# Performance work log

Hardware: AMD Instinct MI355X
Metric: run time of the kernel (lower is better)

## Reference

```python
import jax, jax.numpy as jnp
import numpy as np


def setup_inputs() -> dict:
    key = jax.random.key(0)
    k1, k2 = jax.random.split(key)
    B, Lq, Ls, D = 16, 2048, 2048, 512
    query = jax.random.normal(k1, (B, Lq, D), dtype=jnp.float32)
    support = jax.random.normal(k2, (B, Ls, D), dtype=jnp.float32)
    return {"query": query, "support": support}


def reference(query, support):
    # attn: [B, Lq, Ls] = softmax(query @ support^T, axis=-1)
    logits = jnp.einsum("bqd,bsd->bqs", query, support)
    attn = jax.nn.softmax(logits, axis=-1)
    # attended support: [B, Lq, D]
    attended = jnp.einsum("bqs,bsd->bqd", attn, support)
    # score: [B, Lq] = sum over D of query * attended
    score = jnp.sum(query * attended, axis=-1)
    return score
```

## Files before the change

kernel.cpp:

```cpp
#include <hip/hip_runtime.h>
#include <hip/hip_bf16.h>

#define B_  16
#define LQ  2048
#define LS  2048
#define DD  512
#define BQ  128
#define BS  128
#define BK  64
#define NSB (LS / BS)
#define NKC (DD / BK)
#define NSPLIT 4

typedef short bf16x8 __attribute__((ext_vector_type(8)));
typedef float f32x4  __attribute__((ext_vector_type(4)));

__device__ __forceinline__ void load_lds16(const void* g, void* l) {
  __builtin_amdgcn_global_load_lds((const __attribute__((address_space(1))) void*)g,
                                   (__attribute__((address_space(3))) void*)l,
                                   16, 0, 0);
}

__device__ __forceinline__ unsigned short f2bf(float f) {
  union { float f; unsigned int u; } v; v.f = f;
  unsigned int r = v.u + 0x7fffu + ((v.u >> 16) & 1u);
  return (unsigned short)(r >> 16);
}

__global__ __launch_bounds__(256) void cvt_kernel(const float* __restrict__ Q,
                                                  const float* __restrict__ S,
                                                  unsigned short* __restrict__ Qw,
                                                  unsigned short* __restrict__ Sw,
                                                  int nblk) {
  int blk = blockIdx.x;
  const float* src; unsigned short* dst;
  if (blk < nblk) { src = Q; dst = Qw; } else { src = S; dst = Sw; blk -= nblk; }
  int i = blk * 256 + threadIdx.x;
  float4 f = ((const float4*)src)[i];
  ushort4 u;
  u.x = f2bf(f.x); u.y = f2bf(f.y); u.z = f2bf(f.z); u.w = f2bf(f.w);
  ((ushort4*)dst)[i] = u;
}

__global__ __launch_bounds__(512, 4) void attn_kernel(const unsigned short* __restrict__ Qw,
                                                      const unsigned short* __restrict__ Sw,
                                                      float* __restrict__ out,
                                                      float* __restrict__ pm,
                                                      float* __restrict__ pse,
                                                      float* __restrict__ psel,
                                                      int nsplit) {
  __shared__ __align__(16) unsigned short sQ[BQ * BK];
  __shared__ __align__(16) unsigned short sS[BS * BK];

  const int qb   = blockIdx.x;
  const int b    = blockIdx.y;
  const int spl  = blockIdx.z;
  const int tid  = threadIdx.x;
  const int w    = tid >> 6;
  const int lane = tid & 63;
  const int h    = w & 1;
  const int g    = w >> 1;
  const int col  = lane & 15;
  const int quad = lane >> 4;
  const int c7   = col & 7;

  const int q0 = qb * BQ;
  const unsigned short* Qb = Qw + (size_t)b * LQ * DD;
  const unsigned short* Sb = Sw + (size_t)b * LS * DD;

  float mst[2] = { -INFINITY, -INFINITY };
  float se[2]  = { 0.f, 0.f };
  float sel[2] = { 0.f, 0.f };

  f32x4 acc[4][2];

  const int rr    = lane >> 3;
  const int cc    = ((lane & 7) ^ rr) * 8;
  const int srow0 = (w & 3) * 32;

  const int sbs = spl * (NSB / nsplit);
  const int sbe = sbs + (NSB / nsplit);

  for (int sb = sbs; sb < sbe; ++sb) {
    const int s0 = sb * BS;
#pragma unroll
    for (int st = 0; st < 4; ++st)
#pragma unroll
      for (int qt = 0; qt < 2; ++qt)
        acc[st][qt] = (f32x4){0.f, 0.f, 0.f, 0.f};

    for (int kc = 0; kc < NKC; ++kc) {
      __syncthreads();
      if (w < 4) {
#pragma unroll
        for (int i = 0; i < 4; ++i) {
          int r = srow0 + i * 8 + rr;
          load_lds16(Qb + (size_t)(q0 + r) * DD + kc * BK + cc, &sQ[(srow0 + i * 8) * BK]);
        }
      } else {
#pragma unroll
        for (int i = 0; i < 4; ++i) {
          int r = srow0 + i * 8 + rr;
          load_lds16(Sb + (size_t)(s0 + r) * DD + kc * BK + cc, &sS[(srow0 + i * 8) * BK]);
        }
      }
      __syncthreads();

#pragma unroll
      for (int kk = 0; kk < 2; ++kk) {
        const int koff = ((kk * 4 + quad) ^ c7) * 8;
        bf16x8 aq[2], asv[4];
#pragma unroll
        for (int qt = 0; qt < 2; ++qt)
          aq[qt] = *(const bf16x8*)&sQ[(g * 32 + qt * 16 + col) * BK + koff];
#pragma unroll
        for (int st = 0; st < 4; ++st)
          asv[st] = *(const bf16x8*)&sS[(h * 64 + st * 16 + col) * BK + koff];
#pragma unroll
        for (int st = 0; st < 4; ++st)
#pragma unroll
          for (int qt = 0; qt < 2; ++qt)
            acc[st][qt] = __builtin_amdgcn_mfma_f32_16x16x32_bf16(asv[st], aq[qt], acc[st][qt], 0, 0, 0);
      }
    }

#pragma unroll
    for (int qt = 0; qt < 2; ++qt) {
      float lmax = mst[qt];
#pragma unroll
      for (int st = 0; st < 4; ++st)
#pragma unroll
        for (int r = 0; r < 4; ++r)
          lmax = fmaxf(lmax, acc[st][qt][r]);
      lmax = fmaxf(lmax, __shfl_xor(lmax, 16, 64));
      lmax = fmaxf(lmax, __shfl_xor(lmax, 32, 64));
      float alpha = __expf(mst[qt] - lmax);
      float pe = 0.f, pel = 0.f;
#pragma unroll
      for (int st = 0; st < 4; ++st)
#pragma unroll
        for (int r = 0; r < 4; ++r) {
          float l = acc[st][qt][r];
          float e = __expf(l - lmax);
          pe += e;
          pel = fmaf(e, l, pel);
        }
      pe  += __shfl_xor(pe, 16, 64);  pe  += __shfl_xor(pe, 32, 64);
      pel += __shfl_xor(pel, 16, 64); pel += __shfl_xor(pel, 32, 64);
      se[qt]  = fmaf(se[qt],  alpha, pe);
      sel[qt] = fmaf(sel[qt], alpha, pel);
      mst[qt] = lmax;
    }
  }

  __syncthreads();
  float* red = (float*)sQ;
  if (quad == 0) {
#pragma unroll
    for (int qt = 0; qt < 2; ++qt) {
      int idx = ((g * 2 + h) * 2 + qt) * 16 + col;
      red[idx]       = mst[qt];
      red[256 + idx] = se[qt];
      red[512 + idx] = sel[qt];
    }
  }
  __syncthreads();
  if (h == 0 && quad == 0) {
#pragma unroll
    for (int qt = 0; qt < 2; ++qt) {
      int i0 = ((g * 2 + 0) * 2 + qt) * 16 + col;
      int i1 = ((g * 2 + 1) * 2 + qt) * 16 + col;
      float m0 = red[i0], m1 = red[i1];
      float M  = fmaxf(m0, m1);
      float a0 = __expf(m0 - M), a1 = __expf(m1 - M);
      float SE  = red[256 + i0] * a0 + red[256 + i1] * a1;
      float SEL = red[512 + i0] * a0 + red[512 + i1] * a1;
      size_t qi = (size_t)b * LQ + q0 + g * 32 + qt * 16 + col;
      if (nsplit == 1) {
        out[qi] = SEL / SE;
      } else {
        pm[qi * NSPLIT + spl]   = M;
        pse[qi * NSPLIT + spl]  = SE;
        psel[qi * NSPLIT + spl] = SEL;
      }
    }
  }
}

__global__ __launch_bounds__(256) void combine_kernel(const float* __restrict__ pm,
                                                      const float* __restrict__ pse,
                                                      const float* __restrict__ psel,
                                                      float* __restrict__ out) {
  int i = blockIdx.x * blockDim.x + threadIdx.x;
  if (i >= B_ * LQ) return;
  float M = -INFINITY;
#pragma unroll
  for (int s = 0; s < NSPLIT; ++s) M = fmaxf(M, pm[i * NSPLIT + s]);
  float SE = 0.f, SEL = 0.f;
#pragma unroll
  for (int s = 0; s < NSPLIT; ++s) {
    float a = __expf(pm[i * NSPLIT + s] - M);
    SE  = fmaf(pse[i * NSPLIT + s],  a, SE);
    SEL = fmaf(psel[i * NSPLIT + s], a, SEL);
  }
  out[i] = SEL / SE;
}

__global__ __launch_bounds__(256) void fallback_kernel(const float* __restrict__ Q,
                                                       const float* __restrict__ S,
                                                       float* __restrict__ out) {
  __shared__ float qv[DD];
  __shared__ float red[256];
  const int b = blockIdx.y, qi = blockIdx.x, tid = threadIdx.x;
  const float* qrow = Q + ((size_t)b * LQ + qi) * DD;
  for (int d = tid; d < DD; d += 256) qv[d] = qrow[d];
  __syncthreads();
  const float* Sb = S + (size_t)b * LS * DD;
  float m = -INFINITY, se = 0.f, sel = 0.f;
  for (int s = tid; s < LS; s += 256) {
    const float* srow = Sb + (size_t)s * DD;
    float dot = 0.f;
    for (int d = 0; d < DD; ++d) dot = fmaf(qv[d], srow[d], dot);
    float mn = fmaxf(m, dot);
    float a = __expf(m - mn);
    float e = __expf(dot - mn);
    se  = se * a + e;
    sel = sel * a + e * dot;
    m = mn;
  }
  red[tid] = m; __syncthreads();
  for (int o = 128; o > 0; o >>= 1) { if (tid < o) red[tid] = fmaxf(red[tid], red[tid + o]); __syncthreads(); }
  float M = red[0]; __syncthreads();
  float a = __expf(m - M); se *= a; sel *= a;
  red[tid] = se; __syncthreads();
  for (int o = 128; o > 0; o >>= 1) { if (tid < o) red[tid] += red[tid + o]; __syncthreads(); }
  float SE = red[0]; __syncthreads();
  red[tid] = sel; __syncthreads();
  for (int o = 128; o > 0; o >>= 1) { if (tid < o) red[tid] += red[tid + o]; __syncthreads(); }
  float SEL = red[0];
  if (tid == 0) out[(size_t)b * LQ + qi] = SEL / SE;
}

extern "C" void kernel_launch(void* const* d_in, const int* in_sizes, int n_in,
                              void* d_out, int out_size, void* d_ws, size_t ws_size,
                              hipStream_t stream) {
  const float* Q = (const float*)d_in[0];
  const float* S = (const float*)d_in[1];
  float* out = (float*)d_out;
  const size_t nelem = (size_t)B_ * LQ * DD;
  const size_t need_base  = 2 * nelem * sizeof(unsigned short);
  const size_t part_elems = (size_t)B_ * LQ * NSPLIT;
  const size_t need_split = need_base + 3 * part_elems * sizeof(float);

  if (ws_size >= need_base) {
    unsigned short* Qw = (unsigned short*)d_ws;
    unsigned short* Sw = Qw + nelem;
    int nblk = (int)(nelem / 4 / 256);
    cvt_kernel<<<2 * nblk, 256, 0, stream>>>(Q, S, Qw, Sw, nblk);
    if (ws_size >= need_split) {
      float* pm   = (float*)(Sw + nelem);
      float* pse  = pm + part_elems;
      float* psel = pse + part_elems;
      attn_kernel<<<dim3(LQ / BQ, B_, NSPLIT), 512, 0, stream>>>(Qw, Sw, out, pm, pse, psel, NSPLIT);
      combine_kernel<<<(B_ * LQ + 255) / 256, 256, 0, stream>>>(pm, pse, psel, out);
    } else {
      attn_kernel<<<dim3(LQ / BQ, B_, 1), 512, 0, stream>>>(Qw, Sw, out, nullptr, nullptr, nullptr, 1);
    }
  } else {
    fallback_kernel<<<dim3(LQ, B_), 256, 0, stream>>>(Q, S, out);
  }
}
```

Baseline: 231.2 us.

## Double-buffer LDS tiles and widen support tile to 256 with 1024-thread blocks

Fuses the support-block and k-chunk loops into one flat loop and double-buffers the Q and S tiles in LDS, so the next chunk's global-to-LDS load overlaps the current MFMA work. This removes one of the two barriers per chunk. The support tile grows from 128 to 256 rows with 16 waves per block and the split count drops from 4 to 2. Each Q tile is then reused across more support rows, which cuts redundant Q loads. In exchange LDS use per block doubles and blocks are larger, which may lower occupancy; the grid also halves to 512 blocks.

```diff
diff --git a/kernel.cpp b/kernel.cpp
--- a/kernel.cpp
+++ b/kernel.cpp
@@ -6,11 +6,11 @@
 #define LS  2048
 #define DD  512
 #define BQ  128
-#define BS  128
+#define BS  256
 #define BK  64
 #define NSB (LS / BS)
 #define NKC (DD / BK)
-#define NSPLIT 4
+#define NSPLIT 2
 
 typedef short bf16x8 __attribute__((ext_vector_type(8)));
 typedef float f32x4  __attribute__((ext_vector_type(4)));
@@ -42,15 +42,15 @@
   ((ushort4*)dst)[i] = u;
 }
 
-__global__ __launch_bounds__(512, 4) void attn_kernel(const unsigned short* __restrict__ Qw,
-                                                      const unsigned short* __restrict__ Sw,
-                                                      float* __restrict__ out,
-                                                      float* __restrict__ pm,
-                                                      float* __restrict__ pse,
-                                                      float* __restrict__ psel,
-                                                      int nsplit) {
-  __shared__ __align__(16) unsigned short sQ[BQ * BK];
-  __shared__ __align__(16) unsigned short sS[BS * BK];
+__global__ __launch_bounds__(1024, 4) void attn_kernel(const unsigned short* __restrict__ Qw,
+                                                       const unsigned short* __restrict__ Sw,
+                                                       float* __restrict__ out,
+                                                       float* __restrict__ pm,
+                                                       float* __restrict__ pse,
+                                                       float* __restrict__ psel,
+                                                       int nsplit) {
+  __shared__ __align__(16) unsigned short sQ[2][BQ * BK];
+  __shared__ __align__(16) unsigned short sS[2][BS * BK];
 
   const int qb   = blockIdx.x;
   const int b    = blockIdx.y;
@@ -58,8 +58,8 @@
   const int tid  = threadIdx.x;
   const int w    = tid >> 6;
   const int lane = tid & 63;
-  const int h    = w & 1;
-  const int g    = w >> 1;
+  const int h    = w & 3;
+  const int g    = w >> 2;
   const int col  = lane & 15;
   const int quad = lane >> 4;
   const int c7   = col & 7;
@@ -74,107 +74,113 @@
 
   f32x4 acc[4][2];
 
-  const int rr    = lane >> 3;
-  const int cc    = ((lane & 7) ^ rr) * 8;
-  const int srow0 = (w & 3) * 32;
-
-  const int sbs = spl * (NSB / nsplit);
-  const int sbe = sbs + (NSB / nsplit);
-
-  for (int sb = sbs; sb < sbe; ++sb) {
+  const int rr = lane >> 3;
+  const int cc = ((lane & 7) ^ rr) * 8;
+
+  const int sbp = NSB / nsplit;
+  const int sbs = spl * sbp;
+  const int T   = sbp * NKC;
+
+  auto issue = [&](int t, int buf) {
+    const int sb = sbs + (t >> 3);
+    const int kc = t & 7;
     const int s0 = sb * BS;
-#pragma unroll
-    for (int st = 0; st < 4; ++st)
+    const int kb = kc * BK + cc;
+    load_lds16(Qb + (size_t)(q0 + w * 8 + rr) * DD + kb,        &sQ[buf][(w * 8) * BK]);
+    load_lds16(Sb + (size_t)(s0 + w * 8 + rr) * DD + kb,        &sS[buf][(w * 8) * BK]);
+    load_lds16(Sb + (size_t)(s0 + 128 + w * 8 + rr) * DD + kb,  &sS[buf][(128 + w * 8) * BK]);
+  };
+
+  issue(0, 0);
+
+  for (int t = 0; t < T; ++t) {
+    const int buf = t & 1;
+    __syncthreads();
+    if (t + 1 < T) issue(t + 1, buf ^ 1);
+
+    if ((t & 7) == 0) {
+#pragma unroll
+      for (int st = 0; st < 4; ++st)
+#pragma unroll
+        for (int qt = 0; qt < 2; ++qt)
+          acc[st][qt] = (f32x4){0.f, 0.f, 0.f, 0.f};
+    }
+
+#pragma unroll
+    for (int kk = 0; kk < 2; ++kk) {
+      const int koff = ((kk * 4 + quad) ^ c7) * 8;
+      bf16x8 aq[2], asv[4];
 #pragma unroll
       for (int qt = 0; qt < 2; ++qt)
-        acc[st][qt] = (f32x4){0.f, 0.f, 0.f, 0.f};
-
-    for (int kc = 0; kc < NKC; ++kc) {
-      __syncthreads();
-      if (w < 4) {
-#pragma unroll
-        for (int i = 0; i < 4; ++i) {
-          int r = srow0 + i * 8 + rr;
-          load_lds16(Qb + (size_t)(q0 + r) * DD + kc * BK + cc, &sQ[(srow0 + i * 8) * BK]);
-        }
-      } else {
-#pragma unroll
-        for (int i = 0; i < 4; ++i) {
-          int r = srow0 + i * 8 + rr;
-          load_lds16(Sb + (size_t)(s0 + r) * DD + kc * BK + cc, &sS[(srow0 + i * 8) * BK]);
-        }
+        aq[qt] = *(const bf16x8*)&sQ[buf][(g * 32 + qt * 16 + col) * BK + koff];
+#pragma unroll
+      for (int st = 0; st < 4; ++st)
+        asv[st] = *(const bf16x8*)&sS[buf][(h * 64 + st * 16 + col) * BK + koff];
+#pragma unroll
+      for (int st = 0; st < 4; ++st)
+#pragma unroll
+        for (int qt = 0; qt < 2; ++qt)
+          acc[st][qt] = __builtin_amdgcn_mfma_f32_16x16x32_bf16(asv[st], aq[qt], acc[st][qt], 0, 0, 0);
+    }
+
+    if ((t & 7) == 7) {
+#pragma unroll
+      for (int qt = 0; qt < 2; ++qt) {
+        float lmax = mst[qt];
+#pragma unroll
+        for (int st = 0; st < 4; ++st)
+#pragma unroll
+          for (int r = 0; r < 4; ++r)
+            lmax = fmaxf(lmax, acc[st][qt][r]);
+        lmax = fmaxf(lmax, __shfl_xor(lmax, 16, 64));
+        lmax = fmaxf(lmax, __shfl_xor(lmax, 32, 64));
+        float alpha = __expf(mst[qt] - lmax);
+        float pe = 0.f, pel = 0.f;
+#pragma unroll
+        for (int st = 0; st < 4; ++st)
+#pragma unroll
+          for (int r = 0; r < 4; ++r) {
+            float l = acc[st][qt][r];
+            float e = __expf(l - lmax);
+            pe += e;
+            pel = fmaf(e, l, pel);
+          }
+        pe  += __shfl_xor(pe, 16, 64);  pe  += __shfl_xor(pe, 32, 64);
+        pel += __shfl_xor(pel, 16, 64); pel += __shfl_xor(pel, 32, 64);
+        se[qt]  = fmaf(se[qt],  alpha, pe);
+        sel[qt] = fmaf(sel[qt], alpha, pel);
+        mst[qt] = lmax;
       }
-      __syncthreads();
-
-#pragma unroll
-      for (int kk = 0; kk < 2; ++kk) {
-        const int koff = ((kk * 4 + quad) ^ c7) * 8;
-        bf16x8 aq[2], asv[4];
-#pragma unroll
-        for (int qt = 0; qt < 2; ++qt)
-          aq[qt] = *(const bf16x8*)&sQ[(g * 32 + qt * 16 + col) * BK + koff];
-#pragma unroll
-        for (int st = 0; st < 4; ++st)
-          asv[st] = *(const bf16x8*)&sS[(h * 64 + st * 16 + col) * BK + koff];
-#pragma unroll
-        for (int st = 0; st < 4; ++st)
-#pragma unroll
-          for (int qt = 0; qt < 2; ++qt)
-            acc[st][qt] = __builtin_amdgcn_mfma_f32_16x16x32_bf16(asv[st], aq[qt], acc[st][qt], 0, 0, 0);
-      }
-    }
-
+    }
+  }
+
+  __syncthreads();
+  float* red = (float*)&sQ[0][0];
+  if (quad == 0) {
 #pragma unroll
     for (int qt = 0; qt < 2; ++qt) {
-      float lmax = mst[qt];
-#pragma unroll
-      for (int st = 0; st < 4; ++st)
-#pragma unroll
-        for (int r = 0; r < 4; ++r)
-          lmax = fmaxf(lmax, acc[st][qt][r]);
-      lmax = fmaxf(lmax, __shfl_xor(lmax, 16, 64));
-      lmax = fmaxf(lmax, __shfl_xor(lmax, 32, 64));
-      float alpha = __expf(mst[qt] - lmax);
-      float pe = 0.f, pel = 0.f;
-#pragma unroll
-      for (int st = 0; st < 4; ++st)
-#pragma unroll
-        for (int r = 0; r < 4; ++r) {
-          float l = acc[st][qt][r];
-          float e = __expf(l - lmax);
-          pe += e;
-          pel = fmaf(e, l, pel);
-        }
-      pe  += __shfl_xor(pe, 16, 64);  pe  += __shfl_xor(pe, 32, 64);
-      pel += __shfl_xor(pel, 16, 64); pel += __shfl_xor(pel, 32, 64);
-      se[qt]  = fmaf(se[qt],  alpha, pe);
-      sel[qt] = fmaf(sel[qt], alpha, pel);
-      mst[qt] = lmax;
-    }
-  }
-
-  __syncthreads();
-  float* red = (float*)sQ;
-  if (quad == 0) {
-#pragma unroll
-    for (int qt = 0; qt < 2; ++qt) {
-      int idx = ((g * 2 + h) * 2 + qt) * 16 + col;
-      red[idx]       = mst[qt];
-      red[256 + idx] = se[qt];
-      red[512 + idx] = sel[qt];
+      int idx = ((g * 4 + h) * 2 + qt) * 16 + col;
+      red[idx]        = mst[qt];
+      red[512 + idx]  = se[qt];
+      red[1024 + idx] = sel[qt];
     }
   }
   __syncthreads();
   if (h == 0 && quad == 0) {
 #pragma unroll
     for (int qt = 0; qt < 2; ++qt) {
-      int i0 = ((g * 2 + 0) * 2 + qt) * 16 + col;
-      int i1 = ((g * 2 + 1) * 2 + qt) * 16 + col;
-      float m0 = red[i0], m1 = red[i1];
-      float M  = fmaxf(m0, m1);
-      float a0 = __expf(m0 - M), a1 = __expf(m1 - M);
-      float SE  = red[256 + i0] * a0 + red[256 + i1] * a1;
-      float SEL = red[512 + i0] * a0 + red[512 + i1] * a1;
+      float M = -INFINITY;
+#pragma unroll
+      for (int hh = 0; hh < 4; ++hh)
+        M = fmaxf(M, red[((g * 4 + hh) * 2 + qt) * 16 + col]);
+      float SE = 0.f, SEL = 0.f;
+#pragma unroll
+      for (int hh = 0; hh < 4; ++hh) {
+        int idx = ((g * 4 + hh) * 2 + qt) * 16 + col;
+        float a = __expf(red[idx] - M);
+        SE  = fmaf(red[512 + idx],  a, SE);
+        SEL = fmaf(red[1024 + idx], a, SEL);
+      }
       size_t qi = (size_t)b * LQ + q0 + g * 32 + qt * 16 + col;
       if (nsplit == 1) {
         out[qi] = SEL / SE;
@@ -261,10 +267,10 @@
       float* pm   = (float*)(Sw + nelem);
       float* pse  = pm + part_elems;
       float* psel = pse + part_elems;
-      attn_kernel<<<dim3(LQ / BQ, B_, NSPLIT), 512, 0, stream>>>(Qw, Sw, out, pm, pse, psel, NSPLIT);
+      attn_kernel<<<dim3(LQ / BQ, B_, NSPLIT), 1024, 0, stream>>>(Qw, Sw, out, pm, pse, psel, NSPLIT);
       combine_kernel<<<(B_ * LQ + 255) / 256, 256, 0, stream>>>(pm, pse, psel, out);
     } else {
-      attn_kernel<<<dim3(LQ / BQ, B_, 1), 512, 0, stream>>>(Qw, Sw, out, nullptr, nullptr, nullptr, 1);
+      attn_kernel<<<dim3(LQ / BQ, B_, 1), 1024, 0, stream>>>(Qw, Sw, out, nullptr, nullptr, nullptr, 1);
     }
   } else {
     fallback_kernel<<<dim3(LQ, B_), 256, 0, stream>>>(Q, S, out);
```

Result: slower. 239.7 us (+3.7%).

## Double split-K factor and remap block index so splits share a batch's support in cache

Applied to the files above, without the earlier changes.

Raises the number of support-sequence splits from 4 to 8 and flattens the grid to 1D. Block IDs are decoded so the split index varies fastest, then batch, then query block. Blocks that run at the same time therefore cover different slices of the same batch's support tensor, which should improve L2/MALL reuse and give more blocks to fill the GPU. The cost is twice as much partial-result traffic and a larger combine step. The nsplit==1 path is removed.

```diff
diff --git a/kernel.cpp b/kernel.cpp
--- a/kernel.cpp
+++ b/kernel.cpp
@@ -10,7 +10,7 @@
 #define BK  64
 #define NSB (LS / BS)
 #define NKC (DD / BK)
-#define NSPLIT 4
+#define NSPLIT 8
 
 typedef short bf16x8 __attribute__((ext_vector_type(8)));
 typedef float f32x4  __attribute__((ext_vector_type(4)));
@@ -44,17 +44,16 @@
 
 __global__ __launch_bounds__(512, 4) void attn_kernel(const unsigned short* __restrict__ Qw,
                                                       const unsigned short* __restrict__ Sw,
-                                                      float* __restrict__ out,
                                                       float* __restrict__ pm,
                                                       float* __restrict__ pse,
-                                                      float* __restrict__ psel,
-                                                      int nsplit) {
+                                                      float* __restrict__ psel) {
   __shared__ __align__(16) unsigned short sQ[BQ * BK];
   __shared__ __align__(16) unsigned short sS[BS * BK];
 
-  const int qb   = blockIdx.x;
-  const int b    = blockIdx.y;
-  const int spl  = blockIdx.z;
+  const int id   = blockIdx.x;
+  const int qb   = id >> 7;
+  const int b    = (id >> 3) & 15;
+  const int spl  = id & 7;
   const int tid  = threadIdx.x;
   const int w    = tid >> 6;
   const int lane = tid & 63;
@@ -78,8 +77,9 @@
   const int cc    = ((lane & 7) ^ rr) * 8;
   const int srow0 = (w & 3) * 32;
 
-  const int sbs = spl * (NSB / nsplit);
-  const int sbe = sbs + (NSB / nsplit);
+  const int sbp = NSB / NSPLIT;
+  const int sbs = spl * sbp;
+  const int sbe = sbs + sbp;
 
   for (int sb = sbs; sb < sbe; ++sb) {
     const int s0 = sb * BS;
@@ -176,13 +176,9 @@
       float SE  = red[256 + i0] * a0 + red[256 + i1] * a1;
       float SEL = red[512 + i0] * a0 + red[512 + i1] * a1;
       size_t qi = (size_t)b * LQ + q0 + g * 32 + qt * 16 + col;
-      if (nsplit == 1) {
-        out[qi] = SEL / SE;
-      } else {
-        pm[qi * NSPLIT + spl]   = M;
-        pse[qi * NSPLIT + spl]  = SE;
-        psel[qi * NSPLIT + spl] = SEL;
-      }
+      pm[qi * NSPLIT + spl]   = M;
+      pse[qi * NSPLIT + spl]  = SE;
+      psel[qi * NSPLIT + spl] = SEL;
     }
   }
 }
@@ -248,24 +244,20 @@
   const float* S = (const float*)d_in[1];
   float* out = (float*)d_out;
   const size_t nelem = (size_t)B_ * LQ * DD;
-  const size_t need_base  = 2 * nelem * sizeof(unsigned short);
   const size_t part_elems = (size_t)B_ * LQ * NSPLIT;
-  const size_t need_split = need_base + 3 * part_elems * sizeof(float);
-
-  if (ws_size >= need_base) {
+  const size_t need = 2 * nelem * sizeof(unsigned short)
+                    + 3 * part_elems * sizeof(float);
+
+  if (ws_size >= need) {
     unsigned short* Qw = (unsigned short*)d_ws;
     unsigned short* Sw = Qw + nelem;
+    float* pm   = (float*)(Sw + nelem);
+    float* pse  = pm + part_elems;
+    float* psel = pse + part_elems;
     int nblk = (int)(nelem / 4 / 256);
     cvt_kernel<<<2 * nblk, 256, 0, stream>>>(Q, S, Qw, Sw, nblk);
-    if (ws_size >= need_split) {
-      float* pm   = (float*)(Sw + nelem);
-      float* pse  = pm + part_elems;
-      float* psel = pse + part_elems;
-      attn_kernel<<<dim3(LQ / BQ, B_, NSPLIT), 512, 0, stream>>>(Qw, Sw, out, pm, pse, psel, NSPLIT);
-      combine_kernel<<<(B_ * LQ + 255) / 256, 256, 0, stream>>>(pm, pse, psel, out);
-    } else {
-      attn_kernel<<<dim3(LQ / BQ, B_, 1), 512, 0, stream>>>(Qw, Sw, out, nullptr, nullptr, nullptr, 1);
-    }
+    attn_kernel<<<(LQ / BQ) * B_ * NSPLIT, 512, 0, stream>>>(Qw, Sw, pm, pse, psel);
+    combine_kernel<<<(B_ * LQ + 255) / 256, 256, 0, stream>>>(pm, pse, psel, out);
   } else {
     fallback_kernel<<<dim3(LQ, B_), 256, 0, stream>>>(Q, S, out);
   }
```

Measured after the change: 249.2 us. 7.8% more time.
